# Kernel optimization log

Hardware: AMD Instinct MI355X
Metric: run time of the kernel (lower is better)

The kernel has to match this reference:

```python
import jax, jax.numpy as jnp
import numpy as np

HEADS = 16
DIM_HEAD = 64
EPS = 1e-12  # F.normalize default eps


def setup_inputs() -> dict:
    key = jax.random.key(0)
    k1, k2, k3 = jax.random.split(key, 3)
    b, n, dim = 2, 2048, 1024
    dim_inner = HEADS * DIM_HEAD
    x = jax.random.normal(k1, (b, n, dim), dtype=jnp.float32)
    gamma = jnp.ones((dim,), dtype=jnp.float32)
    w_qkv = jax.random.normal(k2, (dim, 3 * dim_inner), dtype=jnp.float32) * 0.02
    w_out = jax.random.normal(k3, (dim_inner, dim), dtype=jnp.float32) * 0.02
    return {"x": x, "gamma": gamma, "w_qkv": w_qkv, "w_out": w_out}


def reference(x, gamma, w_qkv, w_out):
    b, n, dim = x.shape
    h, d = HEADS, DIM_HEAD
    scale = d ** -0.5

    # RMSNorm (lucidrains): F.normalize(x, dim=-1) * dim**0.5 * gamma
    norm = jnp.sqrt(jnp.sum(x * x, axis=-1, keepdims=True))
    xn = x / jnp.maximum(norm, EPS) * (dim ** 0.5) * gamma

    # qkv projection -> [b, n, 3, h, d] -> q/k/v each [b, h, n, d]
    qkv = (xn @ w_qkv).reshape(b, n, 3, h, d)
    qkv = jnp.transpose(qkv, (2, 0, 3, 1, 4))
    q, k, v = qkv[0], qkv[1], qkv[2]

    q = q * scale
    sim = jnp.einsum('bhid,bhjd->bhij', q, k)  # [b, h, n, n]
    causal_mask = jnp.triu(jnp.ones((n, n), dtype=bool), k=1)
    mask_value = -jnp.finfo(sim.dtype).max
    sim = jnp.where(causal_mask, mask_value, sim)
    attn = jax.nn.softmax(sim, axis=-1)
    out = jnp.einsum('bhij,bhjd->bhid', attn, v)  # [b, h, n, d]

    out = jnp.transpose(out, (0, 2, 1, 3)).reshape(b, n, h * d)
    return out @ w_out
```

## Files before the change

### kernel.cpp

```cpp
#include <hip/hip_runtime.h>

typedef __attribute__((ext_vector_type(8))) short bf16x8;
typedef __attribute__((ext_vector_type(4))) short bf16x4;
typedef __attribute__((ext_vector_type(4))) float f32x4;

static __device__ __forceinline__ short f2bf(float f) {
    union { float f; unsigned u; } v; v.f = f;
    unsigned r = v.u + 0x7fffu + ((v.u >> 16) & 1u);
    return (short)(r >> 16);
}
static __device__ __forceinline__ float bf2f(short s) {
    union { unsigned u; float f; } v; v.u = ((unsigned)(unsigned short)s) << 16;
    return v.f;
}

static __device__ __forceinline__ void async_copy16(const short* g, short* l) {
    __builtin_amdgcn_global_load_lds((const __attribute__((address_space(1))) void*)g,
                                     (__attribute__((address_space(3))) void*)l,
                                     16, 0, 0);
}

#define HEADS 16
#define DHEAD 64
#define NSEQ  2048
#define DIM   1024
#define BATCH 2
#define ROWS  (BATCH * NSEQ)
#define NQKV  (3 * HEADS * DHEAD)

__global__ __launch_bounds__(256) void prep_kernel(const float* __restrict__ x,
                                                   const float* __restrict__ gamma,
                                                   const float* __restrict__ w_qkv,
                                                   const float* __restrict__ w_out,
                                                   short* __restrict__ xn,
                                                   short* __restrict__ wqkvT,
                                                   short* __restrict__ woutT) {
    const int blk = blockIdx.x;
    const int t = threadIdx.x;
    __shared__ float tile[32][33];
    __shared__ float part[4];

    if (blk < 4096) {
        const float* in;  short* out;  int R, C, bx, by;
        if (blk < 3072) { in = w_qkv; out = wqkvT; R = DIM; C = NQKV; bx = blk % 96; by = blk / 96; }
        else            { in = w_out; out = woutT; R = DIM; C = DIM;  bx = (blk - 3072) & 31; by = (blk - 3072) >> 5; }
        const int tx = t & 31, ty = t >> 5;
        const int gx = bx * 32, gy = by * 32;
#pragma unroll
        for (int i = 0; i < 4; ++i)
            tile[ty + i * 8][tx] = in[(size_t)(gy + ty + i * 8) * C + gx + tx];
        __syncthreads();
#pragma unroll
        for (int i = 0; i < 4; ++i)
            out[(size_t)(gx + ty + i * 8) * R + gy + tx] = f2bf(tile[tx][ty + i * 8]);
    } else {
        const int row = blk - 4096;
        const float4 v = ((const float4*)(x + (size_t)row * DIM))[t];
        float s = v.x * v.x + v.y * v.y + v.z * v.z + v.w * v.w;
#pragma unroll
        for (int off = 32; off > 0; off >>= 1) s += __shfl_down(s, off, 64);
        if ((t & 63) == 0) part[t >> 6] = s;
        __syncthreads();
        const float tot = part[0] + part[1] + part[2] + part[3];
        const float scale = 32.0f / fmaxf(sqrtf(tot), 1e-12f);
        const float4 g = ((const float4*)gamma)[t];
        bf16x4 o;
        o[0] = f2bf(v.x * scale * g.x);
        o[1] = f2bf(v.y * scale * g.y);
        o[2] = f2bf(v.z * scale * g.z);
        o[3] = f2bf(v.w * scale * g.w);
        *(bf16x4*)(xn + (size_t)row * DIM + t * 4) = o;
    }
}

template <int MODE, int MT, int NT, int WM, int WN>
__global__ __launch_bounds__(256) void gemm_bt(const short* __restrict__ A,
                                               const short* __restrict__ Bt,
                                               void* __restrict__ Cout,
                                               short* __restrict__ vtOut,
                                               int K, int N) {
    constexpr int TM = WM * MT * 16;
    constexpr int TN = WN * NT * 16;
    __shared__ alignas(16) short lds_a[TM * 32];
    __shared__ alignas(16) short lds_b[TN * 32];
    const int tid = threadIdx.x;
    const int lane = tid & 63, wid = tid >> 6;
    const int quad = lane >> 4, l16 = lane & 15;
    const int wm = wid / WN, wn = wid % WN;
    const int mb = blockIdx.y * TM, nb = blockIdx.x * TN;
    const int ksub = K / gridDim.z;
    const int kbeg = blockIdx.z * ksub;

    f32x4 acc[MT][NT];
#pragma unroll
    for (int i = 0; i < MT; ++i)
#pragma unroll
        for (int j = 0; j < NT; ++j) acc[i][j] = (f32x4){0.f, 0.f, 0.f, 0.f};

    const int lr = lane >> 2;
    const int lc = (lane & 3) * 8;

    for (int kb = kbeg; kb < kbeg + ksub; kb += 32) {
        __syncthreads();
#pragma unroll
        for (int c = 0; c < TM / 64; ++c) {
            const int row = c * 64 + wid * 16 + lr;
            async_copy16(&A[(size_t)(mb + row) * K + kb + lc], &lds_a[row * 32 + lc]);
        }
#pragma unroll
        for (int c = 0; c < TN / 64; ++c) {
            const int row = c * 64 + wid * 16 + lr;
            async_copy16(&Bt[(size_t)(nb + row) * K + kb + lc], &lds_b[row * 32 + lc]);
        }
        __syncthreads();
        bf16x8 af[MT], bfr[NT];
#pragma unroll
        for (int mt = 0; mt < MT; ++mt)
            af[mt] = *(const bf16x8*)&lds_a[(wm * MT * 16 + mt * 16 + l16) * 32 + quad * 8];
#pragma unroll
        for (int nt = 0; nt < NT; ++nt)
            bfr[nt] = *(const bf16x8*)&lds_b[(wn * NT * 16 + nt * 16 + l16) * 32 + quad * 8];
#pragma unroll
        for (int mt = 0; mt < MT; ++mt)
#pragma unroll
            for (int nt = 0; nt < NT; ++nt)
                acc[mt][nt] = __builtin_amdgcn_mfma_f32_16x16x32_bf16(af[mt], bfr[nt],
                                                                      acc[mt][nt], 0, 0, 0);
    }

    const size_t zoff = (size_t)blockIdx.z * ((size_t)gridDim.y * TM) * N;
#pragma unroll
    for (int mt = 0; mt < MT; ++mt) {
#pragma unroll
        for (int nt = 0; nt < NT; ++nt) {
            const int grow0 = mb + wm * MT * 16 + mt * 16 + quad * 4;
            const int gcol  = nb + wn * NT * 16 + nt * 16 + l16;
            if (MODE == 0) {
                const int s3 = gcol >> 10, rem = gcol & 1023;
                const int hh = rem >> 6, dd = rem & 63;
                const int bb = grow0 >> 11, npos0 = grow0 & 2047;
                if (s3 == 2) {
                    bf16x4 vw;
#pragma unroll
                    for (int r = 0; r < 4; ++r) vw[r] = f2bf(acc[mt][nt][r]);
                    *(bf16x4*)&vtOut[((size_t)(bb * 16 + hh) * 64 + dd) * 2048 + npos0] = vw;
                } else {
                    const float sc = (s3 == 0) ? 0.125f : 1.0f;
#pragma unroll
                    for (int r = 0; r < 4; ++r)
                        ((short*)Cout)[(size_t)((s3 * 32 + bb * 16 + hh) * 2048 + npos0 + r) * 64 +
                                       dd] = f2bf(acc[mt][nt][r] * sc);
                }
            } else {
#pragma unroll
                for (int r = 0; r < 4; ++r)
                    ((short*)Cout)[zoff + (size_t)(grow0 + r) * N + gcol] =
                        f2bf(acc[mt][nt][r]);
            }
        }
    }
}

__global__ __launch_bounds__(256) void reduce_kernel(const short* __restrict__ p,
                                                     float* __restrict__ out) {
    const size_t i8 = ((size_t)blockIdx.x * 256 + threadIdx.x) * 8;
    const bf16x8 a = *(const bf16x8*)&p[i8];
    const bf16x8 b = *(const bf16x8*)&p[(size_t)ROWS * DIM + i8];
    float4 o0, o1;
    o0.x = bf2f(a[0]) + bf2f(b[0]);  o0.y = bf2f(a[1]) + bf2f(b[1]);
    o0.z = bf2f(a[2]) + bf2f(b[2]);  o0.w = bf2f(a[3]) + bf2f(b[3]);
    o1.x = bf2f(a[4]) + bf2f(b[4]);  o1.y = bf2f(a[5]) + bf2f(b[5]);
    o1.z = bf2f(a[6]) + bf2f(b[6]);  o1.w = bf2f(a[7]) + bf2f(b[7]);
    *(float4*)&out[i8] = o0;
    *(float4*)&out[i8 + 4] = o1;
}

__global__ __launch_bounds__(256, 3) void attn_kernel(const short* __restrict__ qg,
                                                      const short* __restrict__ kg,
                                                      const short* __restrict__ vtg,
                                                      short* __restrict__ og) {
    const int tid = threadIdx.x;
    const int wid = tid >> 6, lane = tid & 63;
    const int quad = lane >> 4, l16 = lane & 15;
    const int blk = blockIdx.x;
    const int qt = 15 - (blk >> 5);
    const int bh = blk & 31;
    const size_t base = (size_t)bh * (NSEQ * DHEAD);
    const int bb = bh >> 4, hh = bh & 15;
    const int qbase = qt * 128 + wid * 32;
    const int ntiles = 2 * qt + 2;

    __shared__ alignas(16) short kA[2][2048], kB[2][2048];
    __shared__ alignas(16) short vA[2][2048], vB[2][2048];
    __shared__ alignas(16) short pbuf[4][32 * 72];
    short* const pb = pbuf[wid];

    const int sr = tid >> 2;
    const int sc = (tid & 3) * 8;
    auto stage = [&](int t, short (&KB_)[2][2048], short (&VB_)[2][2048]) {
        const int kb = t * 64;
        async_copy16(&kg[base + (size_t)(kb + sr) * 64 + sc],      &KB_[0][sr * 32 + sc]);
        async_copy16(&kg[base + (size_t)(kb + sr) * 64 + 32 + sc], &KB_[1][sr * 32 + sc]);
        async_copy16(&vtg[base + (size_t)sr * 2048 + kb + sc],      &VB_[0][sr * 32 + sc]);
        async_copy16(&vtg[base + (size_t)sr * 2048 + kb + 32 + sc], &VB_[1][sr * 32 + sc]);
    };

    bf16x8 qf[2][2];
#pragma unroll
    for (int qn = 0; qn < 2; ++qn)
#pragma unroll
        for (int kh = 0; kh < 2; ++kh)
            qf[qn][kh] = *(const bf16x8*)&qg[base + (size_t)(qbase + qn * 16 + l16) * DHEAD +
                                            kh * 32 + quad * 8];

    float li[2] = {0.f, 0.f};
    f32x4 accO[2][4];
#pragma unroll
    for (int qn = 0; qn < 2; ++qn)
#pragma unroll
        for (int nc = 0; nc < 4; ++nc) accO[qn][nc] = (f32x4){0.f, 0.f, 0.f, 0.f};

    auto tile_step = [&](const short (&KB_)[2][2048], const short (&VB_)[2][2048], int t) {
        const int kb = t * 64;
        f32x4 sf[2][4];
#pragma unroll
        for (int m = 0; m < 4; ++m) {
            const bf16x8 kf0 = *(const bf16x8*)&KB_[0][(m * 16 + l16) * 32 + quad * 8];
            const bf16x8 kf1 = *(const bf16x8*)&KB_[1][(m * 16 + l16) * 32 + quad * 8];
#pragma unroll
            for (int qn = 0; qn < 2; ++qn) {
                f32x4 z = (f32x4){0.f, 0.f, 0.f, 0.f};
                z = __builtin_amdgcn_mfma_f32_16x16x32_bf16(kf0, qf[qn][0], z, 0, 0, 0);
                sf[qn][m] = __builtin_amdgcn_mfma_f32_16x16x32_bf16(kf1, qf[qn][1], z, 0, 0, 0);
            }
        }
        if (kb + 64 > qbase) {
#pragma unroll
            for (int qn = 0; qn < 2; ++qn) {
                const int myq = qbase + qn * 16 + l16;
#pragma unroll
                for (int m = 0; m < 4; ++m)
#pragma unroll
                    for (int r = 0; r < 4; ++r)
                        if (kb + m * 16 + quad * 4 + r > myq) sf[qn][m][r] = -3.0e38f;
            }
        }
#pragma unroll
        for (int qn = 0; qn < 2; ++qn) {
            float rs = 0.f;
#pragma unroll
            for (int m = 0; m < 4; ++m) {
                bf16x4 pw;
#pragma unroll
                for (int r = 0; r < 4; ++r) {
                    const float p = __expf(sf[qn][m][r]);
                    rs += p;
                    pw[r] = f2bf(p);
                }
                *(bf16x4*)&pb[(qn * 16 + l16) * 72 + m * 16 + quad * 4] = pw;
            }
            li[qn] += rs;
        }
        bf16x8 pf[2][2];
#pragma unroll
        for (int qn = 0; qn < 2; ++qn)
#pragma unroll
            for (int ks = 0; ks < 2; ++ks)
                pf[qn][ks] = *(const bf16x8*)&pb[(qn * 16 + l16) * 72 + ks * 32 + quad * 8];
#pragma unroll
        for (int nc = 0; nc < 4; ++nc) {
            const bf16x8 vf0 = *(const bf16x8*)&VB_[0][(nc * 16 + l16) * 32 + quad * 8];
            const bf16x8 vf1 = *(const bf16x8*)&VB_[1][(nc * 16 + l16) * 32 + quad * 8];
#pragma unroll
            for (int qn = 0; qn < 2; ++qn) {
                accO[qn][nc] = __builtin_amdgcn_mfma_f32_16x16x32_bf16(vf0, pf[qn][0],
                                                                      accO[qn][nc], 0, 0, 0);
                accO[qn][nc] = __builtin_amdgcn_mfma_f32_16x16x32_bf16(vf1, pf[qn][1],
                                                                      accO[qn][nc], 0, 0, 0);
            }
        }
    };

    stage(0, kA, vA);
    __syncthreads();
    for (int t = 0; t < ntiles; t += 2) {
        stage(t + 1, kB, vB);
        tile_step(kA, vA, t);
        __syncthreads();
        if (t + 2 < ntiles) stage(t + 2, kA, vA);
        tile_step(kB, vB, t + 1);
        __syncthreads();
    }

#pragma unroll
    for (int qn = 0; qn < 2; ++qn) {
        li[qn] += __shfl_xor(li[qn], 16, 64);
        li[qn] += __shfl_xor(li[qn], 32, 64);
        const float inv = 1.0f / li[qn];
        const int npos = qbase + qn * 16 + l16;
#pragma unroll
        for (int nc = 0; nc < 4; ++nc) {
            bf16x4 ow;
#pragma unroll
            for (int r = 0; r < 4; ++r) ow[r] = f2bf(accO[qn][nc][r] * inv);
            *(bf16x4*)&og[(size_t)(bb * 2048 + npos) * 1024 + hh * 64 + nc * 16 + quad * 4] = ow;
        }
    }
}

extern "C" void kernel_launch(void* const* d_in, const int* in_sizes, int n_in,
                              void* d_out, int out_size, void* d_ws, size_t ws_size,
                              hipStream_t stream) {
    const float* x     = (const float*)d_in[0];
    const float* gamma = (const float*)d_in[1];
    const float* w_qkv = (const float*)d_in[2];
    const float* w_out = (const float*)d_in[3];
    float* out = (float*)d_out;
    char* ws = (char*)d_ws;

    short* xn     = (short*)(ws);
    short* wqkvT  = (short*)(ws + 8388608);
    short* woutT  = (short*)(ws + 14680064);
    short* q      = (short*)(ws + 16777216);
    short* k      = q + 32 * 2048 * 64;
    short* vt     = k + 32 * 2048 * 64;
    short* attn   = (short*)(ws + 41943040);
    short* part1  = (short*)(ws + 16777216);

    prep_kernel<<<8192, 256, 0, stream>>>(x, gamma, w_qkv, w_out, xn, wqkvT, woutT);
    gemm_bt<0, 4, 4, 2, 2><<<dim3(NQKV / 128, ROWS / 128, 1), 256, 0, stream>>>(xn, wqkvT, q, vt,
                                                                                DIM, NQKV);
    attn_kernel<<<512, 256, 0, stream>>>(q, k, vt, attn);
    gemm_bt<1, 4, 4, 2, 2><<<dim3(DIM / 128, ROWS / 128, 2), 256, 0, stream>>>(attn, woutT, part1,
                                                                               nullptr, DIM, DIM);
    reduce_kernel<<<2048, 256, 0, stream>>>(part1, out);
}
```

Measured before the change: 189.8 us.

## Widen weight transpose tiles, use exp2 softmax, skip fully-masked tiles per warp

The weight transpose in the prep kernel now uses 64x64 tiles with float4 loads and bf16x4 stores, cutting the block count and improving coalescing. The q scale folds in log2(e) so the attention softmax can call exp2f, and P is rounded to bf16 with a cheaper round-half-up conversion. In the attention loop, each wave skips key tiles that lie entirely above its causal diagonal, while still taking part in the shared staging and barriers. The faster bf16 rounding changes results slightly, and waves that skip tiles leave the workgroup unevenly loaded.

```diff
diff --git a/kernel.cpp b/kernel.cpp
--- a/kernel.cpp
+++ b/kernel.cpp
@@ -8,6 +8,10 @@
     union { float f; unsigned u; } v; v.f = f;
     unsigned r = v.u + 0x7fffu + ((v.u >> 16) & 1u);
     return (short)(r >> 16);
+}
+static __device__ __forceinline__ short f2bf_fast(float f) {
+    union { float f; unsigned u; } v; v.f = f;
+    return (short)((v.u + 0x8000u) >> 16);
 }
 static __device__ __forceinline__ float bf2f(short s) {
     union { unsigned u; float f; } v; v.u = ((unsigned)(unsigned short)s) << 16;
@@ -27,6 +31,7 @@
 #define BATCH 2
 #define ROWS  (BATCH * NSEQ)
 #define NQKV  (3 * HEADS * DHEAD)
+#define QSCALE 0.18033688011112042f
 
 __global__ __launch_bounds__(256) void prep_kernel(const float* __restrict__ x,
                                                    const float* __restrict__ gamma,
@@ -37,24 +42,36 @@
                                                    short* __restrict__ woutT) {
     const int blk = blockIdx.x;
     const int t = threadIdx.x;
-    __shared__ float tile[32][33];
+    __shared__ float tile[64][65];
     __shared__ float part[4];
 
-    if (blk < 4096) {
-        const float* in;  short* out;  int R, C, bx, by;
-        if (blk < 3072) { in = w_qkv; out = wqkvT; R = DIM; C = NQKV; bx = blk % 96; by = blk / 96; }
-        else            { in = w_out; out = woutT; R = DIM; C = DIM;  bx = (blk - 3072) & 31; by = (blk - 3072) >> 5; }
-        const int tx = t & 31, ty = t >> 5;
-        const int gx = bx * 32, gy = by * 32;
-#pragma unroll
-        for (int i = 0; i < 4; ++i)
-            tile[ty + i * 8][tx] = in[(size_t)(gy + ty + i * 8) * C + gx + tx];
-        __syncthreads();
-#pragma unroll
-        for (int i = 0; i < 4; ++i)
-            out[(size_t)(gx + ty + i * 8) * R + gy + tx] = f2bf(tile[tx][ty + i * 8]);
+    if (blk < 1024) {
+        const float* in;  short* out;  int C, bx, by;
+        if (blk < 768) { in = w_qkv; out = wqkvT; C = NQKV; bx = blk % 48; by = blk / 48; }
+        else           { in = w_out; out = woutT; C = DIM;  bx = (blk - 768) & 15; by = (blk - 768) >> 4; }
+        const int gx = bx * 64, gy = by * 64;
+        const int lc4 = (t & 15) * 4;
+        const int lr  = t >> 4;
+#pragma unroll
+        for (int p = 0; p < 4; ++p) {
+            const float4 v = *(const float4*)&in[(size_t)(gy + p * 16 + lr) * C + gx + lc4];
+            tile[p * 16 + lr][lc4 + 0] = v.x;
+            tile[p * 16 + lr][lc4 + 1] = v.y;
+            tile[p * 16 + lr][lc4 + 2] = v.z;
+            tile[p * 16 + lr][lc4 + 3] = v.w;
+        }
+        __syncthreads();
+        const int oc  = t >> 2;
+        const int or4 = (t & 3) * 16;
+#pragma unroll
+        for (int j = 0; j < 4; ++j) {
+            bf16x4 w;
+#pragma unroll
+            for (int r = 0; r < 4; ++r) w[r] = f2bf(tile[or4 + j * 4 + r][oc]);
+            *(bf16x4*)&out[(size_t)(gx + oc) * DIM + gy + or4 + j * 4] = w;
+        }
     } else {
-        const int row = blk - 4096;
+        const int row = blk - 1024;
         const float4 v = ((const float4*)(x + (size_t)row * DIM))[t];
         float s = v.x * v.x + v.y * v.y + v.z * v.z + v.w * v.w;
 #pragma unroll
@@ -145,7 +162,7 @@
                     for (int r = 0; r < 4; ++r) vw[r] = f2bf(acc[mt][nt][r]);
                     *(bf16x4*)&vtOut[((size_t)(bb * 16 + hh) * 64 + dd) * 2048 + npos0] = vw;
                 } else {
-                    const float sc = (s3 == 0) ? 0.125f : 1.0f;
+                    const float sc = (s3 == 0) ? QSCALE : 1.0f;
 #pragma unroll
                     for (int r = 0; r < 4; ++r)
                         ((short*)Cout)[(size_t)((s3 * 32 + bb * 16 + hh) * 2048 + npos0 + r) * 64 +
@@ -189,6 +206,7 @@
     const int bb = bh >> 4, hh = bh & 15;
     const int qbase = qt * 128 + wid * 32;
     const int ntiles = 2 * qt + 2;
+    const int wlast = 2 * qt + (wid >> 1);
 
     __shared__ alignas(16) short kA[2][2048], kB[2][2048];
     __shared__ alignas(16) short vA[2][2048], vB[2][2048];
@@ -253,9 +271,9 @@
                 bf16x4 pw;
 #pragma unroll
                 for (int r = 0; r < 4; ++r) {
-                    const float p = __expf(sf[qn][m][r]);
+                    const float p = exp2f(sf[qn][m][r]);
                     rs += p;
-                    pw[r] = f2bf(p);
+                    pw[r] = f2bf_fast(p);
                 }
                 *(bf16x4*)&pb[(qn * 16 + l16) * 72 + m * 16 + quad * 4] = pw;
             }
@@ -285,10 +303,10 @@
     __syncthreads();
     for (int t = 0; t < ntiles; t += 2) {
         stage(t + 1, kB, vB);
-        tile_step(kA, vA, t);
+        if (t <= wlast) tile_step(kA, vA, t);
         __syncthreads();
         if (t + 2 < ntiles) stage(t + 2, kA, vA);
-        tile_step(kB, vB, t + 1);
+        if (t + 1 <= wlast) tile_step(kB, vB, t + 1);
         __syncthreads();
     }
 
@@ -327,7 +345,7 @@
     short* attn   = (short*)(ws + 41943040);
     short* part1  = (short*)(ws + 16777216);
 
-    prep_kernel<<<8192, 256, 0, stream>>>(x, gamma, w_qkv, w_out, xn, wqkvT, woutT);
+    prep_kernel<<<5120, 256, 0, stream>>>(x, gamma, w_qkv, w_out, xn, wqkvT, woutT);
     gemm_bt<0, 4, 4, 2, 2><<<dim3(NQKV / 128, ROWS / 128, 1), 256, 0, stream>>>(xn, wqkvT, q, vt,
                                                                                 DIM, NQKV);
     attn_kernel<<<512, 256, 0, stream>>>(q, k, vt, attn);
```

After: 197.0 us. +3.8%, slower.
